# Kernel tuning notes

Measured on AMD Instinct MI355X. Metric: run time of the kernel, lower is better.

## Reference

```python
import jax, jax.numpy as jnp
import numpy as np

COMMITMENT_COST = 0.25

def setup_inputs() -> dict:
    key = jax.random.key(0)
    k1, k2 = jax.random.split(key)
    B, d_latent = 8192, 512
    ncb, K, d_sub = 2, 8192, 256
    z = jax.random.normal(k1, (B, d_latent), dtype=jnp.float32)
    # original inits uniform(-1/K, 1/K)
    embedding = jax.random.uniform(k2, (ncb, K, d_sub), dtype=jnp.float32,
                                   minval=-1.0 / K, maxval=1.0 / K)
    return {"z": z, "embedding": embedding}


def reference(z, embedding):
    B, d_latent = z.shape
    ncb, K, d_sub = embedding.shape
    z_split = z.reshape(B, ncb, d_sub)

    # squared euclidean distances [B, ncb, K] via ||z||^2 - 2 z.e + ||e||^2
    z_sq = jnp.sum(z_split * z_split, axis=-1)          # [B, ncb]
    e_sq = jnp.sum(embedding * embedding, axis=-1)      # [ncb, K]
    cross = jnp.einsum('bnd,nkd->bnk', z_split, embedding)  # [B, ncb, K]
    distances = z_sq[:, :, None] - 2.0 * cross + e_sq[None, :, :]

    indices = jnp.argmin(distances, axis=-1)            # [B, ncb] int

    # gather quantized vectors: q[b, n] = embedding[n, indices[b, n]]
    cb_ids = jnp.arange(ncb)[None, :]                   # [1, ncb]
    z_q = embedding[cb_ids, indices]                    # [B, ncb, d_sub]

    commitment_loss = COMMITMENT_COST * jnp.mean(
        (z_split - jax.lax.stop_gradient(z_q)) ** 2)
    codebook_loss = jnp.array(0.0, dtype=z.dtype)       # use_ema=True, eval mode

    # straight-through estimator
    z_q_st = z_split + jax.lax.stop_gradient(z_q - z_split)
    quantized = z_q_st.reshape(B, d_latent)

    # perplexity: mean one-hot usage over batch, averaged across codebooks
    counts = jnp.zeros((ncb, K), dtype=z.dtype).at[cb_ids, indices].add(1.0)
    avg_probs = jnp.mean(counts / B, axis=0)            # [K]
    perplexity = jnp.exp(-jnp.sum(avg_probs * jnp.log(avg_probs + 1e-10)))

    return quantized, indices, commitment_loss, codebook_loss, perplexity
```

## Files before the change

kernel.cpp:

```cpp
#include <hip/hip_runtime.h>
#include <hip/hip_fp16.h>


#define KCODES 8192
#define DSUB   256
#define BROWS  8192
#define NROWS  16384
#define NWIN   512

#define QUANT_N  (BROWS * 512)
#define IDX_OFF  QUANT_N
#define LOSS_OFF (QUANT_N + NROWS)

#define WS_ESQ     0
#define WS_ZSQ     65536
#define WS_ZSCL    131072
#define WS_COUNTS  196608
#define WS_WINNER  262144
#define WS_LOSSARR 393216
#define WS_ZQ      1048576
#define WS_EQ8     5242880
#define WS_TM      9437184

#define EPS 2.5e-4f
#define SE_INV (8192.0f * 127.0f)
#define SE (1.0f / SE_INV)


typedef __attribute__((ext_vector_type(4)))  int int4v;
typedef __attribute__((ext_vector_type(16))) int int16v;

__device__ inline void gl2lds16(const void* g, void* l) {
  __builtin_amdgcn_global_load_lds(
      (const __attribute__((address_space(1))) void*)g,
      (__attribute__((address_space(3))) void*)l, 16, 0, 0);
}

__global__ __launch_bounds__(256)
void prep_kernel(const float* __restrict__ z, const float* __restrict__ e,
                 float* __restrict__ e_sq, float* __restrict__ z_sq,
                 float* __restrict__ z_scl,
                 char* __restrict__ zq, char* __restrict__ eq8,
                 int* __restrict__ counts, unsigned long long* __restrict__ winner) {
  int t = blockIdx.x * 256 + threadIdx.x;
  if (t < 16384) { counts[t] = 0; winner[t] = ~0ull; }

  const int w = threadIdx.x >> 6, lane = threadIdx.x & 63;
  const int gi = blockIdx.x * 4 + w;
  const int c32 = lane & 31, l5 = lane >> 5;
  const bool is_e = gi < 512;
  const int n = (gi >> 8) & 1, g = gi & 255;

  const float* src;
  char* dst;
  if (is_e) {
    src = e + ((size_t)(n * KCODES + g * 32 + c32)) * DSUB + l5 * 16;
    dst = eq8 + (size_t)n * 2097152 + (size_t)g * 8192;
  } else {
    src = z + ((size_t)(g * 32 + c32)) * 512 + n * 256 + l5 * 16;
    dst = zq + (size_t)n * 2097152 + (size_t)g * 8192;
  }

  float v[128];
  float ssq = 0.f, mx = 0.f;
  #pragma unroll
  for (int k0 = 0; k0 < 8; ++k0) {
    #pragma unroll
    for (int q = 0; q < 4; ++q) {
      float4 f = *(const float4*)(src + k0 * 32 + q * 4);
      v[k0 * 16 + q * 4 + 0] = f.x; v[k0 * 16 + q * 4 + 1] = f.y;
      v[k0 * 16 + q * 4 + 2] = f.z; v[k0 * 16 + q * 4 + 3] = f.w;
      ssq += f.x * f.x + f.y * f.y + f.z * f.z + f.w * f.w;
      mx = fmaxf(mx, fmaxf(fmaxf(fabsf(f.x), fabsf(f.y)),
                           fmaxf(fabsf(f.z), fabsf(f.w))));
    }
  }
  ssq += __shfl_xor(ssq, 32, 64);
  mx = fmaxf(mx, __shfl_xor(mx, 32, 64));

  float inv;
  if (is_e) {
    inv = SE_INV;
  } else {
    float s = fmaxf(mx, 1e-20f) * (1.0f / 127.0f);
    inv = 1.0f / s;
    if (l5 == 0) z_scl[n * KCODES + g * 32 + c32] = s;
  }

  #pragma unroll
  for (int k0 = 0; k0 < 8; ++k0) {
    uint4 pk;
    unsigned b[4];
    #pragma unroll
    for (int d = 0; d < 4; ++d) {
      unsigned acc = 0;
      #pragma unroll
      for (int j = 0; j < 4; ++j) {
        int q = __float2int_rn(fminf(fmaxf(v[k0 * 16 + d * 4 + j] * inv, -127.f), 127.f));
        acc |= ((unsigned)(q & 255)) << (8 * j);
      }
      b[d] = acc;
    }
    pk.x = b[0]; pk.y = b[1]; pk.z = b[2]; pk.w = b[3];
    *(uint4*)(dst + k0 * 1024 + l5 * 512 + c32 * 16) = pk;
  }

  if (l5 == 0) {
    if (is_e) e_sq[n * KCODES + g * 32 + c32] = ssq;
    else      z_sq[(g * 32 + c32) * 2 + n] = ssq;
  }
}

__global__ __launch_bounds__(256, 2)
void passA_kernel(const char* __restrict__ zq, const char* __restrict__ eq8,
                  const float* __restrict__ e_sq, const float* __restrict__ z_scl,
                  unsigned* __restrict__ tm32, int rowoff) {
  __shared__ char Bs[2][16384];

  const int n    = blockIdx.z;
  const int tid  = threadIdx.x;
  const int w    = tid >> 6, lane = tid & 63;
  const int l5   = lane >> 5, c32 = lane & 31;
  const int cb   = blockIdx.x * 256 + w * 64;
  const int rg   = rowoff + blockIdx.y * 512;

  const char* en = eq8 + (size_t)n * 2097152;
  const char* zn = zq + (size_t)n * 2097152;
  const float* esq = e_sq + n * KCODES;
  const float* zscl = z_scl + n * KCODES;
  unsigned* tmn = tm32 + (size_t)n * (4096 * NWIN);

  const int lo8 = l5 * 512 + c32 * 16;

  int4v areg[8][2];
  #pragma unroll
  for (int k0 = 0; k0 < 8; ++k0)
    #pragma unroll
    for (int mi = 0; mi < 2; ++mi)
      areg[k0][mi] = *(const int4v*)(en + (size_t)((cb >> 5) + mi) * 8192
                                     + k0 * 1024 + lo8);

  float eqv[2][16];
  #pragma unroll
  for (int mi = 0; mi < 2; ++mi)
    #pragma unroll
    for (int reg = 0; reg < 16; ++reg)
      eqv[mi][reg] = esq[cb + mi * 32 + (reg & 3) + 8 * (reg >> 2) + 4 * l5];

  const char* zg = zn + (size_t)(rg >> 5) * 8192;
  #pragma unroll
  for (int i = 0; i < 4; ++i)
    gl2lds16(zg + w * 4096 + i * 1024 + lane * 16, &Bs[0][w * 4096 + i * 1024]);

  for (int nt = 0; nt < 8; ++nt) {
    __syncthreads();
    if (nt < 7) {
      const char* zs = zg + (nt + 1) * 16384;
      char* ld = &Bs[(nt + 1) & 1][0];
      #pragma unroll
      for (int i = 0; i < 4; ++i)
        gl2lds16(zs + w * 4096 + i * 1024 + lane * 16, ld + w * 4096 + i * 1024);
    }
    const char* bsrc = &Bs[nt & 1][0];
    const int rowbase = rg + nt * 64;

    const float s0 = 2.0f * SE * zscl[rowbase + c32];
    const float s1 = 2.0f * SE * zscl[rowbase + 32 + c32];

    int16v acc[2][2];
    #pragma unroll
    for (int mi = 0; mi < 2; ++mi)
      #pragma unroll
      for (int nf = 0; nf < 2; ++nf)
        #pragma unroll
        for (int i = 0; i < 16; ++i) acc[mi][nf][i] = 0;

    #pragma unroll
    for (int k0 = 0; k0 < 8; ++k0) {
      int4v b0 = *(const int4v*)&bsrc[k0 * 1024 + lo8];
      int4v b1 = *(const int4v*)&bsrc[8192 + k0 * 1024 + lo8];
      __builtin_amdgcn_s_setprio(1);
      acc[0][0] = __builtin_amdgcn_mfma_i32_32x32x32_i8(areg[k0][0], b0, acc[0][0], 0, 0, 0);
      acc[0][1] = __builtin_amdgcn_mfma_i32_32x32x32_i8(areg[k0][0], b1, acc[0][1], 0, 0, 0);
      acc[1][0] = __builtin_amdgcn_mfma_i32_32x32x32_i8(areg[k0][1], b0, acc[1][0], 0, 0, 0);
      acc[1][1] = __builtin_amdgcn_mfma_i32_32x32x32_i8(areg[k0][1], b1, acc[1][1], 0, 0, 0);
      __builtin_amdgcn_s_setprio(0);
    }

    #pragma unroll
    for (int nf = 0; nf < 2; ++nf) {
      const float sv = nf ? s1 : s0;
      unsigned wd[4];
      #pragma unroll
      for (int mi = 0; mi < 2; ++mi) {
        float va[16];
        #pragma unroll
        for (int r = 0; r < 16; ++r)
          va[r] = eqv[mi][r] - sv * (float)acc[mi][nf][r];
        float m0 = fminf(fminf(fminf(va[0], va[1]), fminf(va[2], va[3])),
                         fminf(fminf(va[4], va[5]), fminf(va[6], va[7])));
        float m1 = fminf(fminf(fminf(va[8], va[9]), fminf(va[10], va[11])),
                         fminf(fminf(va[12], va[13]), fminf(va[14], va[15])));
        m0 = fminf(m0, __shfl_xor(m0, 32, 64));
        m1 = fminf(m1, __shfl_xor(m1, 32, 64));
        const float t0 = m0 + EPS, t1 = m1 + EPS;
        unsigned a0 = 0, b0m = 0;
        #pragma unroll
        for (int r = 0; r < 8; ++r) {
          const int bp = (r & 3) + 8 * (r >> 2);
          a0  |= (unsigned)(va[r] <= t0) << bp;
          b0m |= (unsigned)(va[r + 8] <= t1) << bp;
        }
        a0 <<= 4 * l5;
        b0m <<= 4 * l5;
        a0  |= (unsigned)__shfl_xor((int)a0, 32, 64);
        b0m |= (unsigned)__shfl_xor((int)b0m, 32, 64);
        wd[mi * 2]     = (unsigned)__half_as_ushort(__float2half(m0)) | (a0 << 16);
        wd[mi * 2 + 1] = (unsigned)__half_as_ushort(__float2half(m1)) | (b0m << 16);
      }
      if (l5 == 0) {
        int zr = rowbase + nf * 32 + c32;
        uint4 o; o.x = wd[0]; o.y = wd[1]; o.z = wd[2]; o.w = wd[3];
        *(uint4*)&tmn[(size_t)(zr - rowoff) * NWIN + (cb >> 4)] = o;
      }
    }
  }
}

__global__ __launch_bounds__(256)
void passB12_kernel(const unsigned* __restrict__ tm32, const float* __restrict__ z,
                    const float* __restrict__ emb, const float* __restrict__ e_sq,
                    const float* __restrict__ z_sq,
                    unsigned long long* __restrict__ winner, int rzoff) {
  __shared__ unsigned buf[4][128];

  const int w = threadIdx.x >> 6, lane = threadIdx.x & 63;
  const int gw = blockIdx.x * 4 + w;
  const int r0 = rzoff + gw * 2;
  const int boff = rzoff >> 1;

  unsigned cnt = 0;
  #pragma unroll
  for (int i = 0; i < 2; ++i) {
    const int rz = r0 + i;
    const int nn = rz & 1, b = rz >> 1;
    const unsigned* p = tm32 + ((size_t)nn * 4096 + (b - boff)) * NWIN + lane * 8;
    uint4 ta = *(const uint4*)p;
    uint4 tb = *(const uint4*)(p + 4);
    unsigned wv[8] = {ta.x, ta.y, ta.z, ta.w, tb.x, tb.y, tb.z, tb.w};
    float v[8];
    #pragma unroll
    for (int j = 0; j < 8; ++j)
      v[j] = __half2float(__ushort_as_half((unsigned short)(wv[j] & 0xFFFFu)));
    float mv = v[0];
    #pragma unroll
    for (int j = 1; j < 8; ++j) mv = fminf(mv, v[j]);
    #pragma unroll
    for (int off = 32; off; off >>= 1) mv = fminf(mv, __shfl_xor(mv, off, 64));
    const float thr = mv + EPS;
    #pragma unroll
    for (int j = 0; j < 8; ++j) {
      unsigned long long mb = __ballot(v[j] <= thr);
      while (mb) {
        int src = __ffsll(mb) - 1;
        mb &= mb - 1;
        unsigned word = (unsigned)__shfl((int)wv[j], src, 64);
        unsigned msk = word >> 16;
        int win = src * 8 + j;
        while (msk) {
          int bit = __ffs(msk) - 1;
          msk &= msk - 1;
          if (cnt < 128) {
            if (lane == 0) buf[w][cnt] = ((unsigned)rz << 13) | (unsigned)(win * 16 + bit);
            ++cnt;
          }
        }
      }
    }
  }
  __syncthreads();

  const int g = lane >> 4, l16 = lane & 15;
  for (unsigned idx = (unsigned)g; idx < cnt; idx += 4) {
    unsigned e = buf[w][idx];
    int rz = (int)(e >> 13), code = (int)(e & 8191u), nn = rz & 1;
    const float4* ep = (const float4*)(emb + ((size_t)nn * KCODES + code) * DSUB);
    const float4* zp = (const float4*)(z + (size_t)rz * DSUB);
    float s = 0.f;
    #pragma unroll
    for (int u = 0; u < 4; ++u) {
      float4 ev = ep[l16 + 16 * u];
      float4 zv = zp[l16 + 16 * u];
      s += ev.x * zv.x; s += ev.y * zv.y; s += ev.z * zv.z; s += ev.w * zv.w;
    }
    s += __shfl_xor(s, 1, 64);
    s += __shfl_xor(s, 2, 64);
    s += __shfl_xor(s, 4, 64);
    s += __shfl_xor(s, 8, 64);
    if (l16 == 0) {
      float bd = (z_sq[rz] - 2.0f * s) + e_sq[nn * KCODES + code];
      atomicMin(&winner[rz],
                ((unsigned long long)__float_as_uint(bd) << 32) | (unsigned)code);
    }
  }
}

__global__ __launch_bounds__(256)
void passB3_kernel(const float* __restrict__ emb,
                   const unsigned long long* __restrict__ winner, float* __restrict__ out,
                   int* __restrict__ counts, float* __restrict__ lossarr) {
  __shared__ float lsum[4];
  const int w = threadIdx.x >> 6, lane = threadIdx.x & 63;
  const int gw = blockIdx.x * 4 + w;
  const int r0 = gw * 4;

  unsigned long long wv[4];
  #pragma unroll
  for (int i = 0; i < 4; ++i) wv[i] = winner[r0 + i];

  float4 ev[4];
  #pragma unroll
  for (int i = 0; i < 4; ++i) {
    int bk = (int)(unsigned)wv[i];
    ev[i] = ((const float4*)(emb + ((size_t)((r0 + i) & 1) * KCODES + bk) * DSUB))[lane];
  }
  #pragma unroll
  for (int i = 0; i < 4; ++i)
    ((float4*)(out + (size_t)(r0 + i) * DSUB))[lane] = ev[i];

  if (lane < 4) {
    int bk = (int)(unsigned)wv[lane];
    out[IDX_OFF + r0 + lane] = (float)bk;
    atomicAdd(&counts[((r0 + lane) & 1) * KCODES + bk], 1);
  }
  if (lane == 0) {
    float ls = 0.f;
    #pragma unroll
    for (int i = 0; i < 4; ++i) ls += __uint_as_float((unsigned)(wv[i] >> 32));
    lsum[w] = ls;
  }
  __syncthreads();
  if (threadIdx.x == 0)
    lossarr[blockIdx.x] = lsum[0] + lsum[1] + lsum[2] + lsum[3];
}

__global__ void final_kernel(const int* __restrict__ counts, const float* __restrict__ lossarr,
                             float* __restrict__ out) {
  __shared__ float redh[256];
  __shared__ float redl[256];
  float h = 0.0f, ls = 0.0f;
  for (int k = threadIdx.x; k < KCODES; k += 256) {
    float p = (float)(counts[k] + counts[KCODES + k]) * (1.0f / 16384.0f);
    h -= p * logf(p + 1e-10f);
  }
  for (int k = threadIdx.x; k < 1024; k += 256) ls += lossarr[k];
  redh[threadIdx.x] = h;
  redl[threadIdx.x] = ls;
  __syncthreads();
  for (int s = 128; s; s >>= 1) {
    if (threadIdx.x < s) {
      redh[threadIdx.x] += redh[threadIdx.x + s];
      redl[threadIdx.x] += redl[threadIdx.x + s];
    }
    __syncthreads();
  }
  if (threadIdx.x == 0) {
    out[LOSS_OFF + 0] = 0.25f * redl[0] * (1.0f / (float)QUANT_N);
    out[LOSS_OFF + 1] = 0.0f;
    out[LOSS_OFF + 2] = expf(redh[0]);
  }
}

extern "C" void kernel_launch(void* const* d_in, const int* in_sizes, int n_in,
                              void* d_out, int out_size, void* d_ws, size_t ws_size,
                              hipStream_t stream) {
  const float* z   = (const float*)d_in[0];
  const float* emb = (const float*)d_in[1];
  float* out = (float*)d_out;
  char*  ws  = (char*)d_ws;

  float* e_sq   = (float*)(ws + WS_ESQ);
  float* z_sq   = (float*)(ws + WS_ZSQ);
  float* z_scl  = (float*)(ws + WS_ZSCL);
  int*   counts = (int*)(ws + WS_COUNTS);
  unsigned long long* winner = (unsigned long long*)(ws + WS_WINNER);
  float* lossarr = (float*)(ws + WS_LOSSARR);
  char* zq  = ws + WS_ZQ;
  char* eq8 = ws + WS_EQ8;
  unsigned* tm32 = (unsigned*)(ws + WS_TM);

  prep_kernel<<<256, 256, 0, stream>>>(z, emb, e_sq, z_sq, z_scl, zq, eq8, counts, winner);
  for (int c = 0; c < 2; ++c) {
    dim3 gA(32, 8, 2);
    passA_kernel<<<gA, 256, 0, stream>>>(zq, eq8, e_sq, z_scl, tm32, c * 4096);
    passB12_kernel<<<1024, 256, 0, stream>>>(tm32, z, emb, e_sq, z_sq, winner, c * 8192);
  }
  passB3_kernel<<<1024, 256, 0, stream>>>(emb, winner, out, counts, lossarr);
  final_kernel<<<1, 256, 0, stream>>>(counts, lossarr, out);
}
```

Before: 170.5 us.

## Fuse histogram and final reduction into gather kernel; coalesce prep loads via LDS

The separate final reduction kernel is merged into the gather kernel. One extra block builds the code-usage histogram in shared memory straight from the winner array and reduces the loss and entropy, so the global counts atomics and the loss array go away. The prep kernel now has each 16-lane group read one full row with coalesced float4 loads instead of holding 128 floats per thread, stages the quantized bytes in LDS, and writes them out contiguously. This saves one launch and lowers register pressure in prep, but the single histogram block runs serially over all 16384 rows and may become the tail of the gather kernel.

```diff
diff --git a/kernel.cpp b/kernel.cpp
--- a/kernel.cpp
+++ b/kernel.cpp
@@ -15,9 +15,7 @@
 #define WS_ESQ     0
 #define WS_ZSQ     65536
 #define WS_ZSCL    131072
-#define WS_COUNTS  196608
 #define WS_WINNER  262144
-#define WS_LOSSARR 393216
 #define WS_ZQ      1048576
 #define WS_EQ8     5242880
 #define WS_TM      9437184
@@ -41,74 +39,73 @@
                  float* __restrict__ e_sq, float* __restrict__ z_sq,
                  float* __restrict__ z_scl,
                  char* __restrict__ zq, char* __restrict__ eq8,
-                 int* __restrict__ counts, unsigned long long* __restrict__ winner) {
+                 unsigned long long* __restrict__ winner) {
+  __shared__ char xfer[4][8192];
   int t = blockIdx.x * 256 + threadIdx.x;
-  if (t < 16384) { counts[t] = 0; winner[t] = ~0ull; }
+  if (t < 16384) winner[t] = ~0ull;
 
   const int w = threadIdx.x >> 6, lane = threadIdx.x & 63;
   const int gi = blockIdx.x * 4 + w;
-  const int c32 = lane & 31, l5 = lane >> 5;
+  const int q = lane >> 4, c = lane & 15;
   const bool is_e = gi < 512;
   const int n = (gi >> 8) & 1, g = gi & 255;
 
-  const float* src;
-  char* dst;
-  if (is_e) {
-    src = e + ((size_t)(n * KCODES + g * 32 + c32)) * DSUB + l5 * 16;
-    dst = eq8 + (size_t)n * 2097152 + (size_t)g * 8192;
-  } else {
-    src = z + ((size_t)(g * 32 + c32)) * 512 + n * 256 + l5 * 16;
-    dst = zq + (size_t)n * 2097152 + (size_t)g * 8192;
-  }
-
-  float v[128];
-  float ssq = 0.f, mx = 0.f;
-  #pragma unroll
-  for (int k0 = 0; k0 < 8; ++k0) {
-    #pragma unroll
-    for (int q = 0; q < 4; ++q) {
-      float4 f = *(const float4*)(src + k0 * 32 + q * 4);
-      v[k0 * 16 + q * 4 + 0] = f.x; v[k0 * 16 + q * 4 + 1] = f.y;
-      v[k0 * 16 + q * 4 + 2] = f.z; v[k0 * 16 + q * 4 + 3] = f.w;
-      ssq += f.x * f.x + f.y * f.y + f.z * f.z + f.w * f.w;
-      mx = fmaxf(mx, fmaxf(fmaxf(fabsf(f.x), fabsf(f.y)),
-                           fmaxf(fabsf(f.z), fabsf(f.w))));
-    }
-  }
-  ssq += __shfl_xor(ssq, 32, 64);
-  mx = fmaxf(mx, __shfl_xor(mx, 32, 64));
-
-  float inv;
-  if (is_e) {
-    inv = SE_INV;
-  } else {
-    float s = fmaxf(mx, 1e-20f) * (1.0f / 127.0f);
-    inv = 1.0f / s;
-    if (l5 == 0) z_scl[n * KCODES + g * 32 + c32] = s;
-  }
-
-  #pragma unroll
-  for (int k0 = 0; k0 < 8; ++k0) {
-    uint4 pk;
-    unsigned b[4];
-    #pragma unroll
-    for (int d = 0; d < 4; ++d) {
+  char* dst = (is_e ? eq8 : zq) + (size_t)n * 2097152 + (size_t)g * 8192;
+
+  #pragma unroll 2
+  for (int i = 0; i < 8; ++i) {
+    const int rr = i * 4 + q;
+    const float* src;
+    if (is_e) src = e + ((size_t)(n * KCODES + g * 32 + rr)) * DSUB;
+    else      src = z + ((size_t)(g * 32 + rr)) * 512 + n * 256;
+
+    float4 f[4];
+    float ssq = 0.f, mx = 0.f;
+    #pragma unroll
+    for (int j = 0; j < 4; ++j) {
+      f[j] = *(const float4*)(src + 4 * c + 64 * j);
+      ssq += f[j].x * f[j].x + f[j].y * f[j].y + f[j].z * f[j].z + f[j].w * f[j].w;
+      mx = fmaxf(mx, fmaxf(fmaxf(fabsf(f[j].x), fabsf(f[j].y)),
+                           fmaxf(fabsf(f[j].z), fabsf(f[j].w))));
+    }
+    #pragma unroll
+    for (int off = 8; off; off >>= 1) {
+      ssq += __shfl_xor(ssq, off, 16);
+      mx = fmaxf(mx, __shfl_xor(mx, off, 16));
+    }
+    float inv, s = 0.f;
+    if (is_e) {
+      inv = SE_INV;
+    } else {
+      s = fmaxf(mx, 1e-20f) * (1.0f / 127.0f);
+      inv = 1.0f / s;
+    }
+    if (c == 0) {
+      if (is_e) {
+        e_sq[n * KCODES + g * 32 + rr] = ssq;
+      } else {
+        z_sq[(g * 32 + rr) * 2 + n] = ssq;
+        z_scl[n * KCODES + g * 32 + rr] = s;
+      }
+    }
+    #pragma unroll
+    for (int j = 0; j < 4; ++j) {
       unsigned acc = 0;
-      #pragma unroll
-      for (int j = 0; j < 4; ++j) {
-        int q = __float2int_rn(fminf(fmaxf(v[k0 * 16 + d * 4 + j] * inv, -127.f), 127.f));
-        acc |= ((unsigned)(q & 255)) << (8 * j);
-      }
-      b[d] = acc;
-    }
-    pk.x = b[0]; pk.y = b[1]; pk.z = b[2]; pk.w = b[3];
-    *(uint4*)(dst + k0 * 1024 + l5 * 512 + c32 * 16) = pk;
-  }
-
-  if (l5 == 0) {
-    if (is_e) e_sq[n * KCODES + g * 32 + c32] = ssq;
-    else      z_sq[(g * 32 + c32) * 2 + n] = ssq;
-  }
+      int q0 = __float2int_rn(fminf(fmaxf(f[j].x * inv, -127.f), 127.f));
+      int q1 = __float2int_rn(fminf(fmaxf(f[j].y * inv, -127.f), 127.f));
+      int q2 = __float2int_rn(fminf(fmaxf(f[j].z * inv, -127.f), 127.f));
+      int q3 = __float2int_rn(fminf(fmaxf(f[j].w * inv, -127.f), 127.f));
+      acc = ((unsigned)(q0 & 255)) | ((unsigned)(q1 & 255) << 8)
+          | ((unsigned)(q2 & 255) << 16) | ((unsigned)(q3 & 255) << 24);
+      const int k = 4 * c + 64 * j;
+      const int off = (k >> 5) * 1024 + ((k >> 4) & 1) * 512 + rr * 16 + (k & 15);
+      *(unsigned*)&xfer[w][off] = acc;
+    }
+  }
+  __syncthreads();
+  #pragma unroll
+  for (int it = 0; it < 8; ++it)
+    *(uint4*)(dst + it * 1024 + lane * 16) = *(const uint4*)&xfer[w][it * 1024 + lane * 16];
 }
 
 __global__ __launch_bounds__(256, 2)
@@ -306,68 +303,70 @@
 }
 
 __global__ __launch_bounds__(256)
-void passB3_kernel(const float* __restrict__ emb,
-                   const unsigned long long* __restrict__ winner, float* __restrict__ out,
-                   int* __restrict__ counts, float* __restrict__ lossarr) {
-  __shared__ float lsum[4];
-  const int w = threadIdx.x >> 6, lane = threadIdx.x & 63;
-  const int gw = blockIdx.x * 4 + w;
-  const int r0 = gw * 4;
-
-  unsigned long long wv[4];
-  #pragma unroll
-  for (int i = 0; i < 4; ++i) wv[i] = winner[r0 + i];
-
-  float4 ev[4];
-  #pragma unroll
-  for (int i = 0; i < 4; ++i) {
-    int bk = (int)(unsigned)wv[i];
-    ev[i] = ((const float4*)(emb + ((size_t)((r0 + i) & 1) * KCODES + bk) * DSUB))[lane];
-  }
-  #pragma unroll
-  for (int i = 0; i < 4; ++i)
-    ((float4*)(out + (size_t)(r0 + i) * DSUB))[lane] = ev[i];
-
-  if (lane < 4) {
-    int bk = (int)(unsigned)wv[lane];
-    out[IDX_OFF + r0 + lane] = (float)bk;
-    atomicAdd(&counts[((r0 + lane) & 1) * KCODES + bk], 1);
-  }
-  if (lane == 0) {
-    float ls = 0.f;
-    #pragma unroll
-    for (int i = 0; i < 4; ++i) ls += __uint_as_float((unsigned)(wv[i] >> 32));
-    lsum[w] = ls;
-  }
-  __syncthreads();
-  if (threadIdx.x == 0)
-    lossarr[blockIdx.x] = lsum[0] + lsum[1] + lsum[2] + lsum[3];
-}
-
-__global__ void final_kernel(const int* __restrict__ counts, const float* __restrict__ lossarr,
-                             float* __restrict__ out) {
-  __shared__ float redh[256];
-  __shared__ float redl[256];
-  float h = 0.0f, ls = 0.0f;
+void passB3F_kernel(const float* __restrict__ emb,
+                    const unsigned long long* __restrict__ winner,
+                    float* __restrict__ out) {
+  __shared__ int hist[KCODES];
+  __shared__ float red[256];
+
+  if (blockIdx.x < 1024) {
+    const int w = threadIdx.x >> 6, lane = threadIdx.x & 63;
+    const int gw = blockIdx.x * 4 + w;
+    const int r0 = gw * 4;
+
+    unsigned long long wv[4];
+    #pragma unroll
+    for (int i = 0; i < 4; ++i) wv[i] = winner[r0 + i];
+
+    float4 ev[4];
+    #pragma unroll
+    for (int i = 0; i < 4; ++i) {
+      int bk = (int)(unsigned)wv[i];
+      ev[i] = ((const float4*)(emb + ((size_t)((r0 + i) & 1) * KCODES + bk) * DSUB))[lane];
+    }
+    #pragma unroll
+    for (int i = 0; i < 4; ++i)
+      ((float4*)(out + (size_t)(r0 + i) * DSUB))[lane] = ev[i];
+
+    if (lane < 4) {
+      out[IDX_OFF + r0 + lane] = (float)(unsigned)(unsigned)wv[lane];
+    }
+    return;
+  }
+
+  for (int k = threadIdx.x; k < KCODES; k += 256) hist[k] = 0;
+  __syncthreads();
+  float ls = 0.f;
+  #pragma unroll 4
+  for (int i = 0; i < 64; ++i) {
+    unsigned long long wv = winner[i * 256 + threadIdx.x];
+    atomicAdd(&hist[(unsigned)wv & 8191u], 1);
+    ls += __uint_as_float((unsigned)(wv >> 32));
+  }
+  __syncthreads();
+  float h = 0.f;
   for (int k = threadIdx.x; k < KCODES; k += 256) {
-    float p = (float)(counts[k] + counts[KCODES + k]) * (1.0f / 16384.0f);
+    float p = (float)hist[k] * (1.0f / 16384.0f);
     h -= p * logf(p + 1e-10f);
   }
-  for (int k = threadIdx.x; k < 1024; k += 256) ls += lossarr[k];
-  redh[threadIdx.x] = h;
-  redl[threadIdx.x] = ls;
+  red[threadIdx.x] = h;
   __syncthreads();
   for (int s = 128; s; s >>= 1) {
-    if (threadIdx.x < s) {
-      redh[threadIdx.x] += redh[threadIdx.x + s];
-      redl[threadIdx.x] += redl[threadIdx.x + s];
-    }
+    if (threadIdx.x < s) red[threadIdx.x] += red[threadIdx.x + s];
     __syncthreads();
   }
+  float hsum = red[0];
+  __syncthreads();
+  red[threadIdx.x] = ls;
+  __syncthreads();
+  for (int s = 128; s; s >>= 1) {
+    if (threadIdx.x < s) red[threadIdx.x] += red[threadIdx.x + s];
+    __syncthreads();
+  }
   if (threadIdx.x == 0) {
-    out[LOSS_OFF + 0] = 0.25f * redl[0] * (1.0f / (float)QUANT_N);
+    out[LOSS_OFF + 0] = 0.25f * red[0] * (1.0f / (float)QUANT_N);
     out[LOSS_OFF + 1] = 0.0f;
-    out[LOSS_OFF + 2] = expf(redh[0]);
+    out[LOSS_OFF + 2] = expf(hsum);
   }
 }
 
@@ -382,19 +381,16 @@
   float* e_sq   = (float*)(ws + WS_ESQ);
   float* z_sq   = (float*)(ws + WS_ZSQ);
   float* z_scl  = (float*)(ws + WS_ZSCL);
-  int*   counts = (int*)(ws + WS_COUNTS);
   unsigned long long* winner = (unsigned long long*)(ws + WS_WINNER);
-  float* lossarr = (float*)(ws + WS_LOSSARR);
   char* zq  = ws + WS_ZQ;
   char* eq8 = ws + WS_EQ8;
   unsigned* tm32 = (unsigned*)(ws + WS_TM);
 
-  prep_kernel<<<256, 256, 0, stream>>>(z, emb, e_sq, z_sq, z_scl, zq, eq8, counts, winner);
+  prep_kernel<<<256, 256, 0, stream>>>(z, emb, e_sq, z_sq, z_scl, zq, eq8, winner);
   for (int c = 0; c < 2; ++c) {
     dim3 gA(32, 8, 2);
     passA_kernel<<<gA, 256, 0, stream>>>(zq, eq8, e_sq, z_scl, tm32, c * 4096);
     passB12_kernel<<<1024, 256, 0, stream>>>(tm32, z, emb, e_sq, z_sq, winner, c * 8192);
   }
-  passB3_kernel<<<1024, 256, 0, stream>>>(emb, winner, out, counts, lossarr);
-  final_kernel<<<1, 256, 0, stream>>>(counts, lossarr, out);
-}
+  passB3F_kernel<<<1025, 256, 0, stream>>>(emb, winner, out);
+}
```

Result: slower. 175.0 us (+2.6%).
